# Kernel tuning notes

Hardware: AMD Instinct MI355X
Metric: run time of the kernel (lower is better)

Reference implementation:

```python
import jax, jax.numpy as jnp
import numpy as np

B = 20000      # batch (edges/nodes)
DIM = 512      # irreps feature dim for x, y, and out
NNZ = 5000     # number of nonzero CG paths


def setup_inputs() -> dict:
    key = jax.random.key(0)
    k1, k2, k3, k4, k5, k6 = jax.random.split(key, 6)
    x = jax.random.normal(k1, (B, DIM), dtype=jnp.float32)
    y = jax.random.normal(k2, (B, DIM), dtype=jnp.float32)
    scale = jax.random.normal(k3, (NNZ,), dtype=jnp.float32)  # CG coefficients
    M = jnp.sort(jax.random.randint(k4, (NNZ,), 0, DIM, dtype=jnp.int32))   # scatter idx into out
    M1 = jax.random.randint(k5, (NNZ,), 0, DIM, dtype=jnp.int32)            # gather idx into x
    M2 = jax.random.randint(k6, (NNZ,), 0, DIM, dtype=jnp.int32)            # gather idx into y
    return {"x": x, "y": y, "scale": scale, "M": M, "M1": M1, "M2": M2}


def reference(x, y, scale, M, M1, M2):
    # sparse_mul: out[b, M[i]] += scale[i] * x[b, M1[i]] * y[b, M2[i]]
    prod = x[:, M1] * y[:, M2] * scale[None, :]          # [B, NNZ]
    out = jnp.zeros((x.shape[0], DIM), dtype=x.dtype)
    out = out.at[:, M].add(prod)                          # scatter-accumulate over feature axis
    return out
```

## Files before the change

### kernel.cpp

```cpp
#include <hip/hip_runtime.h>
#include <hip/hip_fp16.h>


#define BLK    256
#define RROWS  8
#define DIMC   512
#define DEPTH  8
#define SLOTS  256
#define KPAIRS 28
#define CAPS   (2 * KPAIRS - DEPTH)
#define PADKEY 1023



__global__ void prep_sort(const int* __restrict__ M, int nnz,
                          int* __restrict__ hdr, int* __restrict__ sstartG,
                          int4* __restrict__ lanebins)
{
    __shared__ int cnt[DIMC];
    __shared__ int sst[DIMC];
    __shared__ int skey[DIMC];
    __shared__ int wpart[4];
    const int tid = threadIdx.x;

    cnt[tid] = 0; cnt[tid + BLK] = 0;
    __syncthreads();
    for (int i = tid; i < nnz; i += BLK)
        atomicAdd(&cnt[M[i]], 1);
    __syncthreads();

    {
        const int c0 = cnt[2 * tid], c1 = cnt[2 * tid + 1];
        int s = c0 + c1;
        const int lane = tid & 63;
        for (int o = 1; o < 64; o <<= 1) {
            const int up = __shfl_up(s, o, 64);
            if (lane >= o) s += up;
        }
        if (lane == 63) wpart[tid >> 6] = s;
        __syncthreads();
        int off = 0;
        const int w = tid >> 6;
        if (w > 0) off += wpart[0];
        if (w > 1) off += wpart[1];
        if (w > 2) off += wpart[2];
        const int excl = off + s - (c0 + c1);
        sst[2 * tid]     = excl;
        sst[2 * tid + 1] = excl + c0;
        skey[2 * tid]     = (c0 << 10) | (2 * tid);
        skey[2 * tid + 1] = (c1 << 10) | (2 * tid + 1);
    }
    __syncthreads();

    for (int k = 2; k <= DIMC; k <<= 1) {
        for (int j = k >> 1; j > 0; j >>= 1) {
            #pragma unroll
            for (int ii = 0; ii < 2; ++ii) {
                const int i = tid + ii * BLK;
                const int l = i ^ j;
                if (l > i) {
                    const int a = skey[i], b = skey[l];
                    const bool segUp = ((i & k) == 0);
                    if (segUp ? (a < b) : (a > b)) { skey[i] = b; skey[l] = a; }
                }
            }
            __syncthreads();
        }
    }

    {
        const int e1 = skey[tid];
        const int e2 = skey[(DIMC - 1) - tid];
        const int l1 = e1 >> 10, v1 = e1 & 1023;
        const int l2 = e2 >> 10, v2 = e2 & 1023;
        int tot = l1 + l2;
        if (tot > CAPS) tot = CAPS;
        int m = tot;
        for (int o = 32; o > 0; o >>= 1) m = max(m, __shfl_xor(m, o, 64));
        if ((tid & 63) == 0) hdr[tid >> 6] = m;
        lanebins[tid] = make_int4(v1, l1, v2, l2);
        sstartG[tid]       = sst[tid];
        sstartG[tid + BLK] = sst[tid + BLK];
    }
}

__global__ void prep_fill(const float* __restrict__ scale,
                          const int* __restrict__ M1,
                          const int* __restrict__ M2,
                          const int* __restrict__ sstartG,
                          const int4* __restrict__ lanebins,
                          int4* __restrict__ pk2Tp)
{
    const int p   = blockIdx.x;
    const int tid = threadIdx.x;
    const int4 lb = lanebins[tid];
    int2 e[2];
    #pragma unroll
    for (int h = 0; h < 2; ++h) {
        const int k = 2 * p + h;
        int m = PADKEY, idx = -1;
        if (k < lb.y)                 { m = lb.x; idx = sstartG[lb.x] + k; }
        else if ((k - lb.y) < lb.w)   { m = lb.z; idx = sstartG[lb.z] + (k - lb.y); }
        if (idx >= 0)
            e[h] = make_int2(m | (M1[idx] << 10) | (M2[idx] << 20),
                             __float_as_int(scale[idx]));
        else
            e[h] = make_int2(PADKEY, 0);
    }
    pk2Tp[p * BLK + tid] = make_int4(e[0].x, e[0].y, e[1].x, e[1].y);
}

__device__ __forceinline__ void fma8h(const uint4& xu, const uint4& yu,
                                      float s, float4& a0, float4& a1)
{
    const __half2 p0 = __hmul2(*(const __half2*)&xu.x, *(const __half2*)&yu.x);
    const __half2 p1 = __hmul2(*(const __half2*)&xu.y, *(const __half2*)&yu.y);
    const __half2 p2 = __hmul2(*(const __half2*)&xu.z, *(const __half2*)&yu.z);
    const __half2 p3 = __hmul2(*(const __half2*)&xu.w, *(const __half2*)&yu.w);
    a0.x = fmaf(s, __low2float(p0),  a0.x);
    a0.y = fmaf(s, __high2float(p0), a0.y);
    a0.z = fmaf(s, __low2float(p1),  a0.z);
    a0.w = fmaf(s, __high2float(p1), a0.w);
    a1.x = fmaf(s, __low2float(p2),  a1.x);
    a1.y = fmaf(s, __high2float(p2), a1.y);
    a1.z = fmaf(s, __low2float(p3),  a1.z);
    a1.w = fmaf(s, __high2float(p3), a1.w);
}


__global__ __launch_bounds__(BLK, 5) void sparse_mul_t(
    const float* __restrict__ x, const float* __restrict__ y,
    const int* __restrict__ hdr, const int4* __restrict__ pk2Tp,
    float* __restrict__ out, int B)
{
    __shared__ uint4  xs_u[DIMC];
    __shared__ uint4  ys_u[DIMC];
    __shared__ float4 os4[2 * DIMC];

    const int tid = threadIdx.x;
    const int b0  = blockIdx.x * RROWS;
    const bool full = (b0 + RROWS) <= B;

    for (int f = tid; f < 2 * DIMC; f += BLK)
        os4[f] = make_float4(0.f, 0.f, 0.f, 0.f);

    for (int f = tid; f < DIMC; f += BLK) {
        const int d = f;
        float xr[RROWS], yr[RROWS];
        if (full) {
            #pragma unroll
            for (int r = 0; r < RROWS; ++r) {
                xr[r] = x[(size_t)(b0 + r) * DIMC + d];
                yr[r] = y[(size_t)(b0 + r) * DIMC + d];
            }
        } else {
            #pragma unroll
            for (int r = 0; r < RROWS; ++r) {
                const bool ok = (b0 + r) < B;
                xr[r] = ok ? x[(size_t)(b0 + r) * DIMC + d] : 0.f;
                yr[r] = ok ? y[(size_t)(b0 + r) * DIMC + d] : 0.f;
            }
        }
        uint4 xu, yu;
        {
            __half2 h0 = __floats2half2_rn(xr[0], xr[1]);
            __half2 h1 = __floats2half2_rn(xr[2], xr[3]);
            __half2 h2 = __floats2half2_rn(xr[4], xr[5]);
            __half2 h3 = __floats2half2_rn(xr[6], xr[7]);
            xu = make_uint4(*(unsigned*)&h0, *(unsigned*)&h1,
                            *(unsigned*)&h2, *(unsigned*)&h3);
            h0 = __floats2half2_rn(yr[0], yr[1]);
            h1 = __floats2half2_rn(yr[2], yr[3]);
            h2 = __floats2half2_rn(yr[4], yr[5]);
            h3 = __floats2half2_rn(yr[6], yr[7]);
            yu = make_uint4(*(unsigned*)&h0, *(unsigned*)&h1,
                            *(unsigned*)&h2, *(unsigned*)&h3);
        }
        xs_u[d] = xu;
        ys_u[d] = yu;
    }
    __syncthreads();

    {
        const int km = hdr[tid >> 6];
        const int4* pp = pk2Tp + tid;

        int2 buf[DEPTH];
        #pragma unroll
        for (int p = 0; p < DEPTH / 2; ++p) {
            const int4 q = pp[p * BLK];
            buf[2 * p]     = make_int2(q.x, q.y);
            buf[2 * p + 1] = make_int2(q.z, q.w);
        }

        float4 a0 = make_float4(0.f, 0.f, 0.f, 0.f);
        float4 a1 = make_float4(0.f, 0.f, 0.f, 0.f);

        int   mC = buf[0].x & 1023;
        int   sC = buf[0].y;
        uint4 xu = xs_u[((unsigned)buf[0].x >> 10) & 1023u];
        uint4 yu = ys_u[(unsigned)buf[0].x >> 20];
        int   cur = mC;

        for (int k0 = 0; k0 < km; k0 += DEPTH) {
            #pragma unroll
            for (int j = 0; j < DEPTH; ++j) {
                const int2 ne = buf[(j + 1) & (DEPTH - 1)];
                const int   mN  = ne.x & 1023;
                const uint4 xuN = xs_u[((unsigned)ne.x >> 10) & 1023u];
                const uint4 yuN = ys_u[(unsigned)ne.x >> 20];

                if (mC != cur) {
                    os4[2 * cur]     = a0;
                    os4[2 * cur + 1] = a1;
                    a0 = make_float4(0.f, 0.f, 0.f, 0.f);
                    a1 = make_float4(0.f, 0.f, 0.f, 0.f);
                    cur = mC;
                }
                fma8h(xu, yu, __int_as_float(sC), a0, a1);

                if ((j & 1) == 0) {
                    const int4 q = pp[((k0 + DEPTH + j) >> 1) * BLK];
                    buf[j]     = make_int2(q.x, q.y);
                    buf[j + 1] = make_int2(q.z, q.w);
                }
                mC = mN; sC = ne.y; xu = xuN; yu = yuN;
            }
        }
        if (cur != PADKEY) {
            os4[2 * cur]     = a0;
            os4[2 * cur + 1] = a1;
        }
    }
    __syncthreads();

    for (int f = tid; f < DIMC; f += BLK) {
        const int d = f;
        const float4 v0 = os4[2 * d];
        const float4 v1 = os4[2 * d + 1];
        if (full) {
            out[(size_t)(b0 + 0) * DIMC + d] = v0.x;
            out[(size_t)(b0 + 1) * DIMC + d] = v0.y;
            out[(size_t)(b0 + 2) * DIMC + d] = v0.z;
            out[(size_t)(b0 + 3) * DIMC + d] = v0.w;
            out[(size_t)(b0 + 4) * DIMC + d] = v1.x;
            out[(size_t)(b0 + 5) * DIMC + d] = v1.y;
            out[(size_t)(b0 + 6) * DIMC + d] = v1.z;
            out[(size_t)(b0 + 7) * DIMC + d] = v1.w;
        } else {
            const float vv[8] = {v0.x, v0.y, v0.z, v0.w, v1.x, v1.y, v1.z, v1.w};
            #pragma unroll
            for (int r = 0; r < RROWS; ++r)
                if ((b0 + r) < B) out[(size_t)(b0 + r) * DIMC + d] = vv[r];
        }
    }
}


__global__ void prep_r7(const float* __restrict__ scale,
                        const int* __restrict__ M,
                        const int* __restrict__ M1,
                        const int* __restrict__ M2,
                        int2* __restrict__ pk2, int* __restrict__ starts,
                        int nnz)
{
    int i = blockIdx.x * blockDim.x + threadIdx.x;
    if (i < nnz) {
        unsigned key = (unsigned)M[i] | ((unsigned)M1[i] << 10)
                                      | ((unsigned)M2[i] << 20);
        pk2[i] = make_int2((int)key, __float_as_int(scale[i]));
    }
    if (i <= SLOTS) {
        int j = (int)((long long)i * nnz / SLOTS);
        if (j > 0 && j < nnz) {
            const int prev = M[j - 1];
            while (j < nnz && M[j] == prev) ++j;
        }
        if (j > nnz) j = nnz;
        starts[i] = j;
    }
}

__global__ __launch_bounds__(BLK, 5) void sparse_mul_r7(
    const float* __restrict__ x, const float* __restrict__ y,
    const int2* __restrict__ pk2, const int* __restrict__ starts,
    float* __restrict__ out, int B)
{
    __shared__ uint4  xs_u[DIMC];
    __shared__ uint4  ys_u[DIMC];
    __shared__ float4 os4[2 * DIMC];

    const int tid = threadIdx.x;
    const int b0  = blockIdx.x * RROWS;
    const bool full = (b0 + RROWS) <= B;

    for (int f = tid; f < 2 * DIMC; f += BLK)
        os4[f] = make_float4(0.f, 0.f, 0.f, 0.f);

    for (int f = tid; f < DIMC; f += BLK) {
        const int d = f;
        float xr[RROWS], yr[RROWS];
        #pragma unroll
        for (int r = 0; r < RROWS; ++r) {
            const bool ok = full || (b0 + r) < B;
            xr[r] = ok ? x[(size_t)(b0 + r) * DIMC + d] : 0.f;
            yr[r] = ok ? y[(size_t)(b0 + r) * DIMC + d] : 0.f;
        }
        __half2 h0 = __floats2half2_rn(xr[0], xr[1]);
        __half2 h1 = __floats2half2_rn(xr[2], xr[3]);
        __half2 h2 = __floats2half2_rn(xr[4], xr[5]);
        __half2 h3 = __floats2half2_rn(xr[6], xr[7]);
        xs_u[d] = make_uint4(*(unsigned*)&h0, *(unsigned*)&h1,
                             *(unsigned*)&h2, *(unsigned*)&h3);
        h0 = __floats2half2_rn(yr[0], yr[1]);
        h1 = __floats2half2_rn(yr[2], yr[3]);
        h2 = __floats2half2_rn(yr[4], yr[5]);
        h3 = __floats2half2_rn(yr[6], yr[7]);
        ys_u[d] = make_uint4(*(unsigned*)&h0, *(unsigned*)&h1,
                             *(unsigned*)&h2, *(unsigned*)&h3);
    }
    __syncthreads();

    const int i0 = starts[tid];
    const int ie = starts[tid + 1];

    if (i0 < ie) {
        const int last = ie - 1;
        int2 buf[DEPTH];
        #pragma unroll
        for (int j = 0; j < DEPTH; ++j) buf[j] = pk2[min(i0 + j, last)];

        float4 a0 = make_float4(0.f, 0.f, 0.f, 0.f);
        float4 a1 = make_float4(0.f, 0.f, 0.f, 0.f);
        int   mC = buf[0].x & 1023;
        int   sC = buf[0].y;
        uint4 xu = xs_u[((unsigned)buf[0].x >> 10) & 1023u];
        uint4 yu = ys_u[(unsigned)buf[0].x >> 20];
        int   cur = mC;

        for (int base = i0; base < ie; base += DEPTH) {
            #pragma unroll
            for (int j = 0; j < DEPTH; ++j) {
                const int2 ne = buf[(j + 1) & (DEPTH - 1)];
                const int   mN  = ne.x & 1023;
                const uint4 xuN = xs_u[((unsigned)ne.x >> 10) & 1023u];
                const uint4 yuN = ys_u[(unsigned)ne.x >> 20];
                if (mC != cur) {
                    os4[2 * cur]     = a0;
                    os4[2 * cur + 1] = a1;
                    a0 = make_float4(0.f, 0.f, 0.f, 0.f);
                    a1 = make_float4(0.f, 0.f, 0.f, 0.f);
                    cur = mC;
                }
                const float s = (base + j < ie) ? __int_as_float(sC) : 0.f;
                fma8h(xu, yu, s, a0, a1);
                buf[j] = pk2[min(base + DEPTH + j, last)];
                mC = mN; sC = ne.y; xu = xuN; yu = yuN;
            }
        }
        os4[2 * cur]     = a0;
        os4[2 * cur + 1] = a1;
    }
    __syncthreads();

    for (int f = tid; f < DIMC; f += BLK) {
        const int d = f;
        const float4 v0 = os4[2 * d];
        const float4 v1 = os4[2 * d + 1];
        const float vv[8] = {v0.x, v0.y, v0.z, v0.w, v1.x, v1.y, v1.z, v1.w};
        #pragma unroll
        for (int r = 0; r < RROWS; ++r)
            if (full || (b0 + r) < B) out[(size_t)(b0 + r) * DIMC + d] = vv[r];
    }
}

__global__ void sparse_mul_fallback(
    const float* __restrict__ x, const float* __restrict__ y,
    const float* __restrict__ scale, const int* __restrict__ M,
    const int* __restrict__ M1, const int* __restrict__ M2,
    float* __restrict__ out, int nnz)
{
    __shared__ float orow[DIMC];
    const int b = blockIdx.x;
    for (int d = threadIdx.x; d < DIMC; d += blockDim.x) orow[d] = 0.f;
    __syncthreads();
    for (int i = threadIdx.x; i < nnz; i += blockDim.x) {
        const float v = scale[i] * x[(size_t)b * DIMC + M1[i]]
                                 * y[(size_t)b * DIMC + M2[i]];
        atomicAdd(&orow[M[i]], v);
    }
    __syncthreads();
    for (int d = threadIdx.x; d < DIMC; d += blockDim.x)
        out[(size_t)b * DIMC + d] = orow[d];
}

extern "C" void kernel_launch(void* const* d_in, const int* in_sizes, int n_in,
                              void* d_out, int out_size, void* d_ws, size_t ws_size,
                              hipStream_t stream) {
    const float* x     = (const float*)d_in[0];
    const float* y     = (const float*)d_in[1];
    const float* scale = (const float*)d_in[2];
    const int*   M     = (const int*)d_in[3];
    const int*   M1    = (const int*)d_in[4];
    const int*   M2    = (const int*)d_in[5];
    float* out = (float*)d_out;

    const int B   = in_sizes[0] / DIMC;
    const int nnz = in_sizes[2];

    const int grid = (B + RROWS - 1) / RROWS;

    const size_t needT  = 6160 + (size_t)KPAIRS * BLK * sizeof(int4);
    const size_t needR7 = (size_t)nnz * sizeof(int2) + (SLOTS + 1) * sizeof(int);

    if (nnz > 0 && nnz <= 6000 && ws_size >= needT) {
        int*  hdr      = (int*)d_ws;
        int*  sstartG  = (int*)((char*)d_ws + 16);
        int4* lanebins = (int4*)((char*)d_ws + 2064);
        int4* pk2Tp    = (int4*)((char*)d_ws + 6160);
        prep_sort<<<1, BLK, 0, stream>>>(M, nnz, hdr, sstartG, lanebins);
        prep_fill<<<KPAIRS, BLK, 0, stream>>>(scale, M1, M2, sstartG,
                                              lanebins, pk2Tp);
        sparse_mul_t<<<grid, BLK, 0, stream>>>(x, y, hdr, pk2Tp, out, B);
    } else if (nnz > 0 && ws_size >= needR7) {
        int2* pk2   = (int2*)d_ws;
        int* starts = (int*)((char*)d_ws + (size_t)nnz * sizeof(int2));
        const int pn = (nnz > SLOTS + 1) ? nnz : SLOTS + 1;
        prep_r7<<<(pn + BLK - 1) / BLK, BLK, 0, stream>>>(
            scale, M, M1, M2, pk2, starts, nnz);
        sparse_mul_r7<<<grid, BLK, 0, stream>>>(x, y, pk2, starts, out, B);
    } else {
        sparse_mul_fallback<<<B, BLK, 0, stream>>>(x, y, scale, M, M1, M2, out, nnz);
    }
}
```

Before: 155.2 us.

## Make sparse_mul_t persistent, overlapping next-tile staging with previous writeback

Turns the main kernel into a grid-stride persistent kernel capped at 1280 blocks. Each block loops over 8-row tiles. In each iteration it stages the next tile's x/y (converted to fp16) into shared memory while writing back and re-zeroing the previous tile's output. The aim is to cut block launch overhead and to overlap global loads and stores with each other across tiles. The cost is an extra barrier per tile, and with fewer resident blocks latency hiding could get worse.

```diff
diff --git a/kernel.cpp b/kernel.cpp
--- a/kernel.cpp
+++ b/kernel.cpp
@@ -10,6 +10,7 @@
 #define KPAIRS 28
 #define CAPS   (2 * KPAIRS - DEPTH)
 #define PADKEY 1023
+#define GRIDP  1280
 
 
 
@@ -131,60 +132,53 @@
 __global__ __launch_bounds__(BLK, 5) void sparse_mul_t(
     const float* __restrict__ x, const float* __restrict__ y,
     const int* __restrict__ hdr, const int4* __restrict__ pk2Tp,
-    float* __restrict__ out, int B)
+    float* __restrict__ out, int B, int ntiles)
 {
     __shared__ uint4  xs_u[DIMC];
     __shared__ uint4  ys_u[DIMC];
     __shared__ float4 os4[2 * DIMC];
 
     const int tid = threadIdx.x;
-    const int b0  = blockIdx.x * RROWS;
-    const bool full = (b0 + RROWS) <= B;
-
-    for (int f = tid; f < 2 * DIMC; f += BLK)
-        os4[f] = make_float4(0.f, 0.f, 0.f, 0.f);
-
-    for (int f = tid; f < DIMC; f += BLK) {
-        const int d = f;
-        float xr[RROWS], yr[RROWS];
-        if (full) {
-            #pragma unroll
-            for (int r = 0; r < RROWS; ++r) {
-                xr[r] = x[(size_t)(b0 + r) * DIMC + d];
-                yr[r] = y[(size_t)(b0 + r) * DIMC + d];
-            }
-        } else {
-            #pragma unroll
-            for (int r = 0; r < RROWS; ++r) {
-                const bool ok = (b0 + r) < B;
-                xr[r] = ok ? x[(size_t)(b0 + r) * DIMC + d] : 0.f;
-                yr[r] = ok ? y[(size_t)(b0 + r) * DIMC + d] : 0.f;
-            }
-        }
-        uint4 xu, yu;
-        {
+    const int km  = hdr[tid >> 6];
+    const int4* pp = pk2Tp + tid;
+
+    auto STAGE = [&](int tile) {
+        const int b0   = tile * RROWS;
+        const bool full = (b0 + RROWS) <= B;
+        #pragma unroll
+        for (int u = 0; u < 2; ++u) {
+            const int d = tid + u * BLK;
+            float xr[RROWS], yr[RROWS];
+            if (full) {
+                #pragma unroll
+                for (int r = 0; r < RROWS; ++r) {
+                    xr[r] = x[(size_t)(b0 + r) * DIMC + d];
+                    yr[r] = y[(size_t)(b0 + r) * DIMC + d];
+                }
+            } else {
+                #pragma unroll
+                for (int r = 0; r < RROWS; ++r) {
+                    const bool ok = (b0 + r) < B;
+                    xr[r] = ok ? x[(size_t)(b0 + r) * DIMC + d] : 0.f;
+                    yr[r] = ok ? y[(size_t)(b0 + r) * DIMC + d] : 0.f;
+                }
+            }
             __half2 h0 = __floats2half2_rn(xr[0], xr[1]);
             __half2 h1 = __floats2half2_rn(xr[2], xr[3]);
             __half2 h2 = __floats2half2_rn(xr[4], xr[5]);
             __half2 h3 = __floats2half2_rn(xr[6], xr[7]);
-            xu = make_uint4(*(unsigned*)&h0, *(unsigned*)&h1,
-                            *(unsigned*)&h2, *(unsigned*)&h3);
+            xs_u[d] = make_uint4(*(unsigned*)&h0, *(unsigned*)&h1,
+                                 *(unsigned*)&h2, *(unsigned*)&h3);
             h0 = __floats2half2_rn(yr[0], yr[1]);
             h1 = __floats2half2_rn(yr[2], yr[3]);
             h2 = __floats2half2_rn(yr[4], yr[5]);
             h3 = __floats2half2_rn(yr[6], yr[7]);
-            yu = make_uint4(*(unsigned*)&h0, *(unsigned*)&h1,
-                            *(unsigned*)&h2, *(unsigned*)&h3);
-        }
-        xs_u[d] = xu;
-        ys_u[d] = yu;
-    }
-    __syncthreads();
-
-    {
-        const int km = hdr[tid >> 6];
-        const int4* pp = pk2Tp + tid;
-
+            ys_u[d] = make_uint4(*(unsigned*)&h0, *(unsigned*)&h1,
+                                 *(unsigned*)&h2, *(unsigned*)&h3);
+        }
+    };
+
+    auto PATH = [&]() {
         int2 buf[DEPTH];
         #pragma unroll
         for (int p = 0; p < DEPTH / 2; ++p) {
@@ -231,29 +225,59 @@
             os4[2 * cur]     = a0;
             os4[2 * cur + 1] = a1;
         }
-    }
-    __syncthreads();
-
-    for (int f = tid; f < DIMC; f += BLK) {
-        const int d = f;
-        const float4 v0 = os4[2 * d];
-        const float4 v1 = os4[2 * d + 1];
-        if (full) {
-            out[(size_t)(b0 + 0) * DIMC + d] = v0.x;
-            out[(size_t)(b0 + 1) * DIMC + d] = v0.y;
-            out[(size_t)(b0 + 2) * DIMC + d] = v0.z;
-            out[(size_t)(b0 + 3) * DIMC + d] = v0.w;
-            out[(size_t)(b0 + 4) * DIMC + d] = v1.x;
-            out[(size_t)(b0 + 5) * DIMC + d] = v1.y;
-            out[(size_t)(b0 + 6) * DIMC + d] = v1.z;
-            out[(size_t)(b0 + 7) * DIMC + d] = v1.w;
-        } else {
-            const float vv[8] = {v0.x, v0.y, v0.z, v0.w, v1.x, v1.y, v1.z, v1.w};
-            #pragma unroll
-            for (int r = 0; r < RROWS; ++r)
-                if ((b0 + r) < B) out[(size_t)(b0 + r) * DIMC + d] = vv[r];
-        }
-    }
+    };
+
+    auto WRITEBACK = [&](int tile, bool rezero) {
+        const int b0   = tile * RROWS;
+        const bool full = (b0 + RROWS) <= B;
+        #pragma unroll
+        for (int u = 0; u < 2; ++u) {
+            const int d = tid + u * BLK;
+            const float4 v0 = os4[2 * d];
+            const float4 v1 = os4[2 * d + 1];
+            if (rezero) {
+                os4[2 * d]     = make_float4(0.f, 0.f, 0.f, 0.f);
+                os4[2 * d + 1] = make_float4(0.f, 0.f, 0.f, 0.f);
+            }
+            if (full) {
+                out[(size_t)(b0 + 0) * DIMC + d] = v0.x;
+                out[(size_t)(b0 + 1) * DIMC + d] = v0.y;
+                out[(size_t)(b0 + 2) * DIMC + d] = v0.z;
+                out[(size_t)(b0 + 3) * DIMC + d] = v0.w;
+                out[(size_t)(b0 + 4) * DIMC + d] = v1.x;
+                out[(size_t)(b0 + 5) * DIMC + d] = v1.y;
+                out[(size_t)(b0 + 6) * DIMC + d] = v1.z;
+                out[(size_t)(b0 + 7) * DIMC + d] = v1.w;
+            } else {
+                const float vv[8] = {v0.x, v0.y, v0.z, v0.w,
+                                     v1.x, v1.y, v1.z, v1.w};
+                #pragma unroll
+                for (int r = 0; r < RROWS; ++r)
+                    if ((b0 + r) < B) out[(size_t)(b0 + r) * DIMC + d] = vv[r];
+            }
+        }
+    };
+
+    int tile = blockIdx.x;
+    if (tile >= ntiles) return;
+
+    for (int f = tid; f < 2 * DIMC; f += BLK)
+        os4[f] = make_float4(0.f, 0.f, 0.f, 0.f);
+    STAGE(tile);
+    __syncthreads();
+    PATH();
+
+    int prev = tile;
+    for (tile += gridDim.x; tile < ntiles; tile += gridDim.x) {
+        __syncthreads();
+        STAGE(tile);
+        WRITEBACK(prev, true);
+        __syncthreads();
+        PATH();
+        prev = tile;
+    }
+    __syncthreads();
+    WRITEBACK(prev, false);
 }
 
 
@@ -408,7 +432,7 @@
     const int B   = in_sizes[0] / DIMC;
     const int nnz = in_sizes[2];
 
-    const int grid = (B + RROWS - 1) / RROWS;
+    const int ntiles = (B + RROWS - 1) / RROWS;
 
     const size_t needT  = 6160 + (size_t)KPAIRS * BLK * sizeof(int4);
     const size_t needR7 = (size_t)nnz * sizeof(int2) + (SLOTS + 1) * sizeof(int);
@@ -421,14 +445,15 @@
         prep_sort<<<1, BLK, 0, stream>>>(M, nnz, hdr, sstartG, lanebins);
         prep_fill<<<KPAIRS, BLK, 0, stream>>>(scale, M1, M2, sstartG,
                                               lanebins, pk2Tp);
-        sparse_mul_t<<<grid, BLK, 0, stream>>>(x, y, hdr, pk2Tp, out, B);
+        const int grid = ntiles < GRIDP ? ntiles : GRIDP;
+        sparse_mul_t<<<grid, BLK, 0, stream>>>(x, y, hdr, pk2Tp, out, B, ntiles);
     } else if (nnz > 0 && ws_size >= needR7) {
         int2* pk2   = (int2*)d_ws;
         int* starts = (int*)((char*)d_ws + (size_t)nnz * sizeof(int2));
         const int pn = (nnz > SLOTS + 1) ? nnz : SLOTS + 1;
         prep_r7<<<(pn + BLK - 1) / BLK, BLK, 0, stream>>>(
             scale, M, M1, M2, pk2, starts, nnz);
-        sparse_mul_r7<<<grid, BLK, 0, stream>>>(x, y, pk2, starts, out, B);
+        sparse_mul_r7<<<ntiles, BLK, 0, stream>>>(x, y, pk2, starts, out, B);
     } else {
         sparse_mul_fallback<<<B, BLK, 0, stream>>>(x, y, scale, M, M1, M2, out, nnz);
     }
```

After: 155.0 us. About the same (-0.2%).
